# Kernel tuning notes

Hardware: AMD Instinct MI355X
Metric: run time of the kernel (lower is better)

The kernel has to match this reference:

```python
import jax, jax.numpy as jnp
import numpy as np

B, S, D_MODEL, D_HIDDEN = 4, 2048, 1024, 4096

# --- BitNet b1.58-style quantizers (STE in bwd version) ---

def act_quant(x):
    # per-token int8 absmax quantization over last dim
    scale = 127.0 / jnp.clip(jnp.max(jnp.abs(x), axis=-1, keepdims=True), 1e-5)
    return jnp.clip(jnp.round(x * scale), -128, 127) / scale

def weight_quant(w):
    # ternary weights with global mean-abs scale
    scale = 1.0 / jnp.clip(jnp.mean(jnp.abs(w)), 1e-5)
    return jnp.clip(jnp.round(w * scale), -1, 1) / scale

def bit_linear(x, w):
    # STE: forward uses quantized values, gradient passes through
    xq = x + jax.lax.stop_gradient(act_quant(x) - x)
    wq = w + jax.lax.stop_gradient(weight_quant(w) - w)
    return jnp.einsum('bsd,hd->bsh', xq, wq)

def depthwise_conv1d(x_bcl, w, b):
    # x_bcl: [B, C, L], w: [C, 1, 3], b: [C]
    y = jax.lax.conv_general_dilated(
        x_bcl, w, window_strides=(1,), padding=[(1, 1)],
        dimension_numbers=('NCH', 'OIH', 'NCH'),
        feature_group_count=x_bcl.shape[1])
    return y + b[None, :, None]


def setup_inputs() -> dict:
    key = jax.random.key(0)
    ks = jax.random.split(key, 5)
    lim1 = 1.0 / np.sqrt(D_MODEL)
    lim2 = 1.0 / np.sqrt(D_HIDDEN)
    limc = 1.0 / np.sqrt(3.0)  # fan_in = 1*3 for depthwise conv
    return {
        'x': jax.random.normal(ks[0], (B, S, D_MODEL), dtype=jnp.float32),
        'w1': jax.random.uniform(ks[1], (D_HIDDEN, D_MODEL), jnp.float32, -lim1, lim1),
        'conv_w': jax.random.uniform(ks[2], (D_HIDDEN, 1, 3), jnp.float32, -limc, limc),
        'conv_b': jax.random.uniform(ks[3], (D_HIDDEN,), jnp.float32, -limc, limc),
        'w2': jax.random.uniform(ks[4], (D_MODEL, D_HIDDEN), jnp.float32, -lim2, lim2),
    }


def reference(x, w1, conv_w, conv_b, w2):
    h = bit_linear(x, w1)                      # [B, S, H]
    h = depthwise_conv1d(h.transpose(0, 2, 1), conv_w, conv_b)  # [B, H, S]
    h = h.transpose(0, 2, 1)                   # [B, S, H]
    h = jax.nn.silu(h)
    return bit_linear(h, w2)                   # [B, S, D]
```

## Files before the change

kernel.cpp:

```cpp
#include <hip/hip_runtime.h>
#include <cstdint>

#define S_    2048
#define DM    1024
#define DH    4096
#define NTOK  8192
#define WELEM 4194304
#define CT    8
#define NS    3

typedef int v4i __attribute__((ext_vector_type(4)));
typedef _Float16 half8 __attribute__((ext_vector_type(8)));
typedef char char8v __attribute__((ext_vector_type(8)));

#define GLOAD_LDS16(g, l)                                                   \
    __builtin_amdgcn_global_load_lds(                                       \
        (const __attribute__((address_space(1))) void*)(g),                 \
        (__attribute__((address_space(3))) void*)(l), 16, 0, 0)

#define WAITCNT_VM16  0x4F70
#define WAITCNT_VM0   0x0F70
#define WAITCNT_LGKM0 0xC07F

__global__ __launch_bounds__(256) void absmean_partial(const float4* __restrict__ wa,
                                                       const float4* __restrict__ wb,
                                                       double* __restrict__ partial) {
    __shared__ double red[256];
    const float4* w = (blockIdx.x < 1024) ? wa : wb;
    int base = (blockIdx.x & 1023) * 1024;
    double s = 0.0;
#pragma unroll
    for (int k = 0; k < 4; ++k) {
        float4 v = w[base + (k << 8) + threadIdx.x];
        s += (double)fabsf(v.x) + (double)fabsf(v.y) +
             (double)fabsf(v.z) + (double)fabsf(v.w);
    }
    red[threadIdx.x] = s;
    __syncthreads();
    for (int off = 128; off > 0; off >>= 1) {
        if (threadIdx.x < off) red[threadIdx.x] += red[threadIdx.x + off];
        __syncthreads();
    }
    if (threadIdx.x == 0) partial[blockIdx.x] = red[0];
}

__global__ __launch_bounds__(256) void finalize_scales(const double* __restrict__ part,
                                                       float* __restrict__ sc) {
    __shared__ double red[1024];
#pragma unroll 1
    for (int m = 0; m < 2; ++m) {
        const double* p = part + m * 1024;
        __syncthreads();
#pragma unroll
        for (int k = 0; k < 4; ++k) red[(k << 8) + threadIdx.x] = p[(k << 8) + threadIdx.x];
        __syncthreads();
        double s = red[threadIdx.x] + red[threadIdx.x + 256] +
                   red[threadIdx.x + 512] + red[threadIdx.x + 768];
        __syncthreads();
        red[threadIdx.x] = s;
        __syncthreads();
        for (int off = 128; off > 0; off >>= 1) {
            if (threadIdx.x < off) red[threadIdx.x] += red[threadIdx.x + off];
            __syncthreads();
        }
        if (threadIdx.x == 0) {
            double mean = red[0] / (double)WELEM;
            float mf = fmaxf((float)mean, 1e-5f);
            float scale = 1.0f / mf;
            sc[2 * m]     = scale;
            sc[2 * m + 1] = 1.0f / scale;
        }
    }
}

__global__ __launch_bounds__(256) void quant_all(const float4* __restrict__ w1,
                                                 const float4* __restrict__ w2,
                                                 const float4* __restrict__ x,
                                                 char4* __restrict__ qw1,
                                                 char4* __restrict__ qw2,
                                                 char4* __restrict__ qx,
                                                 float* __restrict__ dqx,
                                                 const float* __restrict__ sc) {
    __shared__ float red[256];
    if (blockIdx.x < 8192) {
        bool second = blockIdx.x >= 4096;
        const float4* w = second ? w2 : w1;
        char4* q = second ? qw2 : qw1;
        float scale = sc[second ? 2 : 0];
        int i = (blockIdx.x & 4095) * 256 + threadIdx.x;
        float4 v = w[i];
        char4 o;
        o.x = (signed char)(int)fminf(fmaxf(rintf(v.x * scale), -1.f), 1.f);
        o.y = (signed char)(int)fminf(fmaxf(rintf(v.y * scale), -1.f), 1.f);
        o.z = (signed char)(int)fminf(fmaxf(rintf(v.z * scale), -1.f), 1.f);
        o.w = (signed char)(int)fminf(fmaxf(rintf(v.w * scale), -1.f), 1.f);
        q[i] = o;
    } else {
        int t = blockIdx.x - 8192;
        float4 v = x[(size_t)t * 256 + threadIdx.x];
        float mx = fmaxf(fmaxf(fabsf(v.x), fabsf(v.y)), fmaxf(fabsf(v.z), fabsf(v.w)));
        red[threadIdx.x] = mx;
        __syncthreads();
        for (int off = 128; off > 0; off >>= 1) {
            if (threadIdx.x < off) red[threadIdx.x] = fmaxf(red[threadIdx.x], red[threadIdx.x + off]);
            __syncthreads();
        }
        float scale = 127.0f / fmaxf(red[0], 1e-5f);
        char4 o;
        o.x = (signed char)(int)fminf(fmaxf(rintf(v.x * scale), -128.f), 127.f);
        o.y = (signed char)(int)fminf(fmaxf(rintf(v.y * scale), -128.f), 127.f);
        o.z = (signed char)(int)fminf(fmaxf(rintf(v.z * scale), -128.f), 127.f);
        o.w = (signed char)(int)fminf(fmaxf(rintf(v.w * scale), -128.f), 127.f);
        qx[(size_t)t * 256 + threadIdx.x] = o;
        if (threadIdx.x == 0) dqx[t] = 1.0f / scale;
    }
}

__global__ __launch_bounds__(512) void conv_silu_quant(const half8* __restrict__ h,
                                                       const float4* __restrict__ cwv,
                                                       const float4* __restrict__ cbv,
                                                       char8v* __restrict__ q,
                                                       float* __restrict__ dq) {
    __shared__ float red[2][8];
    const int tid = threadIdx.x;
    const int t0 = blockIdx.x * CT;
    const int s0 = t0 & (S_ - 1);

    float wc[24], bs[8];
    {
        float4 tmp;
#pragma unroll
        for (int i = 0; i < 6; ++i) {
            tmp = cwv[tid * 6 + i];
            wc[4 * i] = tmp.x; wc[4 * i + 1] = tmp.y; wc[4 * i + 2] = tmp.z; wc[4 * i + 3] = tmp.w;
        }
        tmp = cbv[tid * 2];     bs[0] = tmp.x; bs[1] = tmp.y; bs[2] = tmp.z; bs[3] = tmp.w;
        tmp = cbv[tid * 2 + 1]; bs[4] = tmp.x; bs[5] = tmp.y; bs[6] = tmp.z; bs[7] = tmp.w;
    }

    auto ldrow = [&](int t, bool valid, float* dst) {
        if (valid) {
            half8 raw = h[(size_t)t * 512 + tid];
#pragma unroll
            for (int e = 0; e < 8; ++e) dst[e] = (float)raw[e];
        } else {
#pragma unroll
            for (int e = 0; e < 8; ++e) dst[e] = 0.f;
        }
    };

    float pv[8], cu[8], nx[8], pf[8];
    ldrow(t0 - 1, s0 > 0, pv);
    ldrow(t0, true, cu);
    ldrow(t0 + 1, true, nx);

#pragma unroll
    for (int i = 0; i < CT; ++i) {
        const int t = t0 + i;
        ldrow(t + 2, (s0 + i + 2) < S_, pf);

        float v[8];
        float mx = 0.f;
#pragma unroll
        for (int e = 0; e < 8; ++e) {
            float y = wc[3 * e] * pv[e] + wc[3 * e + 1] * cu[e] + wc[3 * e + 2] * nx[e] + bs[e];
            float r = y / (1.0f + expf(-y));
            v[e] = r;
            mx = fmaxf(mx, fabsf(r));
        }
#pragma unroll
        for (int off = 32; off > 0; off >>= 1)
            mx = fmaxf(mx, __shfl_down(mx, off, 64));
        if ((tid & 63) == 0) red[i & 1][tid >> 6] = mx;
        __syncthreads();
        float rmax = red[i & 1][0];
#pragma unroll
        for (int w = 1; w < 8; ++w) rmax = fmaxf(rmax, red[i & 1][w]);
        float scale = 127.0f / fmaxf(rmax, 1e-5f);
        char8v o;
#pragma unroll
        for (int e = 0; e < 8; ++e)
            o[e] = (signed char)(int)fminf(fmaxf(rintf(v[e] * scale), -128.f), 127.f);
        q[(size_t)t * 512 + tid] = o;
        if (tid == 0) dq[t] = 1.0f / scale;
#pragma unroll
        for (int e = 0; e < 8; ++e) { pv[e] = cu[e]; cu[e] = nx[e]; nx[e] = pf[e]; }
    }
}

template <typename OutT>
__global__ __launch_bounds__(320) void gemm_i8_pc(const int8_t* __restrict__ A,
                                                  const int8_t* __restrict__ Bm,
                                                  OutT* __restrict__ C,
                                                  const float* __restrict__ rowdq,
                                                  const float* __restrict__ sc, int slot,
                                                  int N, int K) {
    __shared__ __align__(16) int8_t Alds[NS][8192];
    __shared__ __align__(16) int8_t Blds[NS][8192];
    __shared__ int flag[NS];
    __shared__ int cnt[NS];
    const int tid  = threadIdx.x;
    const int lane = tid & 63;
    const int wave = tid >> 6;
    const int mbase = blockIdx.y << 7;
    const int nbase = blockIdx.x << 7;
    const int niter = K >> 6;

    if (tid < NS) { flag[tid] = 0; cnt[tid] = 0; }
    __syncthreads();

    if (wave == 4) {
        const int r_l = lane >> 2;
        const int c_l = ((lane & 3) - ((lane >> 3) & 3)) & 3;
        const int8_t* Agb = A  + (size_t)(mbase + r_l) * K + c_l * 16;
        const int8_t* Bgb = Bm + (size_t)(nbase + r_l) * K + c_l * 16;
        const size_t ts = (size_t)16 * K;

        auto issue = [&](int j) {
            const int s = j % NS;
            const int k0 = j << 6;
#pragma unroll
            for (int t = 0; t < 8; ++t)
                GLOAD_LDS16(Agb + (size_t)t * ts + k0, &Alds[s][t << 10]);
#pragma unroll
            for (int t = 0; t < 8; ++t)
                GLOAD_LDS16(Bgb + (size_t)t * ts + k0, &Blds[s][t << 10]);
        };

        issue(0);
        if (niter > 1) issue(1);
        for (int it = 0; it < niter; ++it) {
            if (it + 1 < niter) __builtin_amdgcn_s_waitcnt(WAITCNT_VM16);
            else                __builtin_amdgcn_s_waitcnt(WAITCNT_VM0);
            __hip_atomic_store(&flag[it % NS], it + 1,
                               __ATOMIC_RELAXED, __HIP_MEMORY_SCOPE_WORKGROUP);
            const int j = it + 2;
            if (j < niter) {
                const int s2 = j % NS, need = 4 * (j / NS);
                while (__hip_atomic_load(&cnt[s2], __ATOMIC_RELAXED,
                                         __HIP_MEMORY_SCOPE_WORKGROUP) < need)
                    __builtin_amdgcn_s_sleep(1);
                issue(j);
            }
        }
        return;
    }

    const int wm4 = (wave >> 1) << 2;
    const int wn4 = (wave & 1) << 2;
    const int m_l = lane & 15, q_l = lane >> 4;
    const int fro = (4 * m_l + ((q_l + (m_l >> 1)) & 3)) << 4;

    v4i acc[4][4] = {};
    for (int it = 0; it < niter; ++it) {
        const int s = it % NS;
        while (__hip_atomic_load(&flag[s], __ATOMIC_ACQUIRE,
                                 __HIP_MEMORY_SCOPE_WORKGROUP) < it + 1)
            __builtin_amdgcn_s_sleep(1);
        v4i af[4], bf[4];
#pragma unroll
        for (int i = 0; i < 4; ++i)
            af[i] = *reinterpret_cast<const v4i*>(&Alds[s][fro + ((wm4 + i) << 10)]);
#pragma unroll
        for (int j = 0; j < 4; ++j)
            bf[j] = *reinterpret_cast<const v4i*>(&Blds[s][fro + ((wn4 + j) << 10)]);
        __builtin_amdgcn_s_waitcnt(WAITCNT_LGKM0);
        if (lane == 0)
            __hip_atomic_fetch_add(&cnt[s], 1, __ATOMIC_RELAXED,
                                   __HIP_MEMORY_SCOPE_WORKGROUP);
#pragma unroll
        for (int i = 0; i < 4; ++i)
#pragma unroll
            for (int j = 0; j < 4; ++j)
                acc[i][j] = __builtin_amdgcn_mfma_i32_16x16x64_i8(af[i], bf[j], acc[i][j], 0, 0, 0);
    }

    const float wdq = sc[slot];
    const int quad = lane >> 4;
    const int col  = lane & 15;
#pragma unroll
    for (int i = 0; i < 4; ++i) {
#pragma unroll
        for (int r = 0; r < 4; ++r) {
            int m = mbase + ((wm4 + i) << 4) + (quad << 2) + r;
            float rs = rowdq[m] * wdq;
#pragma unroll
            for (int j = 0; j < 4; ++j) {
                int n = nbase + ((wn4 + j) << 4) + col;
                C[(size_t)m * N + n] = (OutT)((float)acc[i][j][r] * rs);
            }
        }
    }
}

extern "C" void kernel_launch(void* const* d_in, const int* in_sizes, int n_in,
                              void* d_out, int out_size, void* d_ws, size_t ws_size,
                              hipStream_t stream) {
    const float* x  = (const float*)d_in[0];
    const float* w1 = (const float*)d_in[1];
    const float* cw = (const float*)d_in[2];
    const float* cb = (const float*)d_in[3];
    const float* w2 = (const float*)d_in[4];
    float* out = (float*)d_out;
    char* ws = (char*)d_ws;

    double* part  = (double*)(ws + 0);
    float*  sc    = (float*)(ws + 16384);
    float*  dqx   = (float*)(ws + 16640);
    float*  dqh   = (float*)(ws + 49408);
    int8_t* qw1   = (int8_t*)(ws + 82176);
    int8_t* qw2   = (int8_t*)(ws + 4276480);
    int8_t* qx    = (int8_t*)(ws + 8470784);
    int8_t* qh    = (int8_t*)(ws + 16859392);
    _Float16* h   = (_Float16*)(ws + 50413824);

    absmean_partial<<<2048, 256, 0, stream>>>((const float4*)w1, (const float4*)w2, part);
    finalize_scales<<<1, 256, 0, stream>>>(part, sc);
    quant_all<<<16384, 256, 0, stream>>>((const float4*)w1, (const float4*)w2,
                                         (const float4*)x, (char4*)qw1, (char4*)qw2,
                                         (char4*)qx, dqx, sc);

    dim3 g1(DH / 128, NTOK / 128);
    gemm_i8_pc<_Float16><<<g1, 320, 0, stream>>>(qx, qw1, h, dqx, sc, 1, DH, DM);

    conv_silu_quant<<<NTOK / CT, 512, 0, stream>>>((const half8*)h, (const float4*)cw,
                                                   (const float4*)cb, (char8v*)qh, dqh);

    dim3 g2(DM / 128, NTOK / 128);
    gemm_i8_pc<float><<<g2, 320, 0, stream>>>(qh, qw2, out, dqh, sc, 3, DM, DH);
}
```

Before: 274.5 us.

## Replace producer-wave int8 GEMM with barrier-synchronised 256x128 triple-buffered pipeline

Rewrites the int8 GEMM so that it no longer relies on a dedicated loader wave plus LDS flag and counter spin-waits. All eight waves now issue async global-to-LDS loads into a three-stage ring, synchronised with s_barrier and explicit vmcnt waits. The block tile grows to 256x128 with a K-step of 128, and an XOR-swizzled LDS layout is meant to avoid bank conflicts. The aim is to raise MFMA utilisation and remove the spin-loop overhead. The cost is much more LDS per block (144KB), which limits occupancy to about one block per CU despite launch_bounds(512,2).

New measurement: 257.5 us. -6.2%, faster.

```diff
diff --git a/kernel.cpp b/kernel.cpp
--- a/kernel.cpp
+++ b/kernel.cpp
@@ -7,7 +7,6 @@
 #define NTOK  8192
 #define WELEM 4194304
 #define CT    8
-#define NS    3
 
 typedef int v4i __attribute__((ext_vector_type(4)));
 typedef _Float16 half8 __attribute__((ext_vector_type(8)));
@@ -18,9 +17,14 @@
         (const __attribute__((address_space(1))) void*)(g),                 \
         (__attribute__((address_space(3))) void*)(l), 16, 0, 0)
 
-#define WAITCNT_VM16  0x4F70
-#define WAITCNT_VM0   0x0F70
-#define WAITCNT_LGKM0 0xC07F
+static __device__ __forceinline__ void sbar() {
+    asm volatile("" ::: "memory");
+    __builtin_amdgcn_s_barrier();
+    asm volatile("" ::: "memory");
+}
+#define LGKM0() asm volatile("s_waitcnt lgkmcnt(0)" ::: "memory")
+#define VMC6()  asm volatile("s_waitcnt vmcnt(6)" ::: "memory")
+#define VMC0()  asm volatile("s_waitcnt vmcnt(0)" ::: "memory")
 
 __global__ __launch_bounds__(256) void absmean_partial(const float4* __restrict__ wa,
                                                        const float4* __restrict__ wb,
@@ -189,90 +193,100 @@
 }
 
 template <typename OutT>
-__global__ __launch_bounds__(320) void gemm_i8_pc(const int8_t* __restrict__ A,
-                                                  const int8_t* __restrict__ Bm,
-                                                  OutT* __restrict__ C,
-                                                  const float* __restrict__ rowdq,
-                                                  const float* __restrict__ sc, int slot,
-                                                  int N, int K) {
-    __shared__ __align__(16) int8_t Alds[NS][8192];
-    __shared__ __align__(16) int8_t Blds[NS][8192];
-    __shared__ int flag[NS];
-    __shared__ int cnt[NS];
+__global__ __launch_bounds__(512, 2) void gemm_i8_3s(const int8_t* __restrict__ A,
+                                                     const int8_t* __restrict__ Bm,
+                                                     OutT* __restrict__ C,
+                                                     const float* __restrict__ rowdq,
+                                                     const float* __restrict__ sc, int slot,
+                                                     int N, int K) {
+    __shared__ __align__(16) int8_t lds[3][49152];
     const int tid  = threadIdx.x;
     const int lane = tid & 63;
     const int wave = tid >> 6;
-    const int mbase = blockIdx.y << 7;
+    const int mbase = blockIdx.y << 8;
     const int nbase = blockIdx.x << 7;
-    const int niter = K >> 6;
-
-    if (tid < NS) { flag[tid] = 0; cnt[tid] = 0; }
-    __syncthreads();
-
-    if (wave == 4) {
-        const int r_l = lane >> 2;
-        const int c_l = ((lane & 3) - ((lane >> 3) & 3)) & 3;
-        const int8_t* Agb = A  + (size_t)(mbase + r_l) * K + c_l * 16;
-        const int8_t* Bgb = Bm + (size_t)(nbase + r_l) * K + c_l * 16;
-        const size_t ts = (size_t)16 * K;
-
-        auto issue = [&](int j) {
-            const int s = j % NS;
-            const int k0 = j << 6;
-#pragma unroll
-            for (int t = 0; t < 8; ++t)
-                GLOAD_LDS16(Agb + (size_t)t * ts + k0, &Alds[s][t << 10]);
-#pragma unroll
-            for (int t = 0; t < 8; ++t)
-                GLOAD_LDS16(Bgb + (size_t)t * ts + k0, &Blds[s][t << 10]);
-        };
-
-        issue(0);
-        if (niter > 1) issue(1);
-        for (int it = 0; it < niter; ++it) {
-            if (it + 1 < niter) __builtin_amdgcn_s_waitcnt(WAITCNT_VM16);
-            else                __builtin_amdgcn_s_waitcnt(WAITCNT_VM0);
-            __hip_atomic_store(&flag[it % NS], it + 1,
-                               __ATOMIC_RELAXED, __HIP_MEMORY_SCOPE_WORKGROUP);
-            const int j = it + 2;
-            if (j < niter) {
-                const int s2 = j % NS, need = 4 * (j / NS);
-                while (__hip_atomic_load(&cnt[s2], __ATOMIC_RELAXED,
-                                         __HIP_MEMORY_SCOPE_WORKGROUP) < need)
-                    __builtin_amdgcn_s_sleep(1);
-                issue(j);
-            }
-        }
-        return;
-    }
-
-    const int wm4 = (wave >> 1) << 2;
-    const int wn4 = (wave & 1) << 2;
-    const int m_l = lane & 15, q_l = lane >> 4;
-    const int fro = (4 * m_l + ((q_l + (m_l >> 1)) & 3)) << 4;
+    const int NT = K >> 7;
+
+    const int wm = wave >> 1;
+    const int wn = wave & 1;
+
+    const int srow  = tid >> 3;
+    const int lchnk = (tid & 7) ^ (srow & 7);
+    const int8_t* Ag = A  + (size_t)(mbase + srow) * K + (lchnk << 4);
+    const int8_t* Bg = Bm + (size_t)(nbase + srow) * K + (lchnk << 4);
+    const size_t rstep = (size_t)64 * K;
+
+    auto stage = [&](int s, int t, int half) {
+        const size_t ko = (size_t)t << 7;
+        int8_t* db = &lds[s][wave << 10];
+        if (half == 0) {
+            GLOAD_LDS16(Ag + ko,               db);
+            GLOAD_LDS16(Ag + ko + rstep,       db + 8192);
+            GLOAD_LDS16(Ag + ko + 2 * rstep,   db + 16384);
+        } else {
+            GLOAD_LDS16(Ag + ko + 3 * rstep,   db + 24576);
+            GLOAD_LDS16(Bg + ko,               db + 32768);
+            GLOAD_LDS16(Bg + ko + rstep,       db + 40960);
+        }
+    };
+
+    const int fc0 = (((lane >> 4)    ) ^ (lane & 7)) << 4;
+    const int fc1 = (((lane >> 4) | 4) ^ (lane & 7)) << 4;
+    const int aro = ((wm << 6) + (lane & 15)) << 7;
+    const int bro = 32768 + (((wn << 6) + (lane & 15)) << 7);
 
     v4i acc[4][4] = {};
-    for (int it = 0; it < niter; ++it) {
-        const int s = it % NS;
-        while (__hip_atomic_load(&flag[s], __ATOMIC_ACQUIRE,
-                                 __HIP_MEMORY_SCOPE_WORKGROUP) < it + 1)
-            __builtin_amdgcn_s_sleep(1);
+
+    stage(0, 0, 0); stage(0, 0, 1);
+    if (NT > 1) { stage(1, 1, 0); stage(1, 1, 1); }
+    if (NT > 1) VMC6(); else VMC0();
+    sbar();
+
+    int sb = 0;
+    for (int t = 0; t < NT; ++t) {
+        const int8_t* base = &lds[sb][0];
+        int s2 = sb + 2; if (s2 >= 3) s2 -= 3;
+
         v4i af[4], bf[4];
 #pragma unroll
         for (int i = 0; i < 4; ++i)
-            af[i] = *reinterpret_cast<const v4i*>(&Alds[s][fro + ((wm4 + i) << 10)]);
+            af[i] = *reinterpret_cast<const v4i*>(base + aro + (i << 11) + fc0);
 #pragma unroll
         for (int j = 0; j < 4; ++j)
-            bf[j] = *reinterpret_cast<const v4i*>(&Blds[s][fro + ((wn4 + j) << 10)]);
-        __builtin_amdgcn_s_waitcnt(WAITCNT_LGKM0);
-        if (lane == 0)
-            __hip_atomic_fetch_add(&cnt[s], 1, __ATOMIC_RELAXED,
-                                   __HIP_MEMORY_SCOPE_WORKGROUP);
+            bf[j] = *reinterpret_cast<const v4i*>(base + bro + (j << 11) + fc0);
+        if (t + 2 < NT) stage(s2, t + 2, 0);
+        sbar();
+        LGKM0();
+        __builtin_amdgcn_s_setprio(1);
 #pragma unroll
         for (int i = 0; i < 4; ++i)
 #pragma unroll
             for (int j = 0; j < 4; ++j)
                 acc[i][j] = __builtin_amdgcn_mfma_i32_16x16x64_i8(af[i], bf[j], acc[i][j], 0, 0, 0);
+        __builtin_amdgcn_s_setprio(0);
+        sbar();
+
+#pragma unroll
+        for (int i = 0; i < 4; ++i)
+            af[i] = *reinterpret_cast<const v4i*>(base + aro + (i << 11) + fc1);
+#pragma unroll
+        for (int j = 0; j < 4; ++j)
+            bf[j] = *reinterpret_cast<const v4i*>(base + bro + (j << 11) + fc1);
+        if (t + 2 < NT) stage(s2, t + 2, 1);
+        sbar();
+        LGKM0();
+        __builtin_amdgcn_s_setprio(1);
+#pragma unroll
+        for (int i = 0; i < 4; ++i)
+#pragma unroll
+            for (int j = 0; j < 4; ++j)
+                acc[i][j] = __builtin_amdgcn_mfma_i32_16x16x64_i8(af[i], bf[j], acc[i][j], 0, 0, 0);
+        __builtin_amdgcn_s_setprio(0);
+        if (t + 2 < NT)      VMC6();
+        else if (t + 1 < NT) VMC0();
+        sbar();
+
+        if (++sb == 3) sb = 0;
     }
 
     const float wdq = sc[slot];
@@ -282,11 +296,11 @@
     for (int i = 0; i < 4; ++i) {
 #pragma unroll
         for (int r = 0; r < 4; ++r) {
-            int m = mbase + ((wm4 + i) << 4) + (quad << 2) + r;
+            int m = mbase + (wm << 6) + (i << 4) + (quad << 2) + r;
             float rs = rowdq[m] * wdq;
 #pragma unroll
             for (int j = 0; j < 4; ++j) {
-                int n = nbase + ((wn4 + j) << 4) + col;
+                int n = nbase + (wn << 6) + (j << 4) + col;
                 C[(size_t)m * N + n] = (OutT)((float)acc[i][j][r] * rs);
             }
         }
@@ -320,12 +334,12 @@
                                          (const float4*)x, (char4*)qw1, (char4*)qw2,
                                          (char4*)qx, dqx, sc);
 
-    dim3 g1(DH / 128, NTOK / 128);
-    gemm_i8_pc<_Float16><<<g1, 320, 0, stream>>>(qx, qw1, h, dqx, sc, 1, DH, DM);
+    dim3 g1(DH / 128, NTOK / 256);
+    gemm_i8_3s<_Float16><<<g1, 512, 0, stream>>>(qx, qw1, h, dqx, sc, 1, DH, DM);
 
     conv_silu_quant<<<NTOK / CT, 512, 0, stream>>>((const half8*)h, (const float4*)cw,
                                                    (const float4*)cb, (char8v*)qh, dqh);
 
-    dim3 g2(DM / 128, NTOK / 128);
-    gemm_i8_pc<float><<<g2, 320, 0, stream>>>(qh, qw2, out, dqh, sc, 3, DM, DH);
-}
+    dim3 g2(DM / 128, NTOK / 256);
+    gemm_i8_3s<float><<<g2, 512, 0, stream>>>(qh, qw2, out, dqh, sc, 3, DM, DH);
+}
```
